# Kernel tuning notes

Hardware: AMD Instinct MI355X
Metric: run time of the kernel (lower is better)

The kernel has to match this reference:

```python
import jax, jax.numpy as jnp
import numpy as np

IN_FEATURES = 4096
OUT_FEATURES = 4096
BATCH = 4096
MASK_DENSITY = 0.05  # typical power-grid neighborhood sparsity


def setup_inputs() -> dict:
    key = jax.random.key(0)
    k_x, k_w, k_b, k_m = jax.random.split(key, 4)
    x = jax.random.normal(k_x, (BATCH, IN_FEATURES), dtype=jnp.float32)
    # kaiming_uniform_(a=sqrt(5)) -> uniform(-bound, bound), bound = sqrt(6/((1+5)*fan_in)) = 1/sqrt(fan_in)
    w_bound = 1.0 / np.sqrt(IN_FEATURES)
    weight = jax.random.uniform(k_w, (OUT_FEATURES, IN_FEATURES), dtype=jnp.float32,
                                minval=-w_bound, maxval=w_bound)
    bias = jax.random.uniform(k_b, (OUT_FEATURES,), dtype=jnp.float32,
                              minval=-w_bound, maxval=w_bound)
    # fixed binary neighborhood filter (non-trainable), int-valued {0,1} as in the torch module
    myFilter = (jax.random.uniform(k_m, (OUT_FEATURES, IN_FEATURES)) < MASK_DENSITY).astype(jnp.float32)
    return {"x": x, "weight": weight, "bias": bias, "myFilter": myFilter}


def reference(x, weight, bias, myFilter):
    # F.linear(input, weight * myFilter, bias): y = x @ (W * M)^T + b
    masked_w = weight * myFilter                      # [out, in]
    return jnp.einsum('bi,oi->bo', x, masked_w) + bias  # [batch, out]
```

## Files before the change

### kernel.cpp

```cpp
#include <hip/hip_runtime.h>
#include <hip/hip_bf16.h>
#include <stdint.h>

#define IN_F   4096
#define OUT_F  4096
#define BATCH  4096

typedef __bf16 bf16x8_t __attribute__((ext_vector_type(8)));
typedef float  f32x4_t  __attribute__((ext_vector_type(4)));
typedef float  f32x4v   __attribute__((ext_vector_type(4)));
typedef unsigned short u16x4v __attribute__((ext_vector_type(4)));

#define AS_GLOBAL(p) ((const __attribute__((address_space(1))) void*)(p))
#define AS_LDS(p)    ((__attribute__((address_space(3))) void*)(p))

__device__ __forceinline__ unsigned short f32_to_bf16_rne(float f) {
    union { float f; uint32_t u; } v; v.f = f;
    uint32_t u = v.u;
    u += 0x7FFFu + ((u >> 16) & 1u);
    return (unsigned short)(u >> 16);
}

__global__ __launch_bounds__(256)
void convert_kernel(const float* __restrict__ x,
                    const float* __restrict__ w,
                    const float* __restrict__ m,
                    unsigned short* __restrict__ xb,
                    unsigned short* __restrict__ wb) {
    const int64_t i0 = (int64_t)blockIdx.x * 512 + threadIdx.x;
#pragma unroll
    for (int u = 0; u < 2; ++u) {
        const int64_t i = i0 + u * 256;
        f32x4v xv = __builtin_nontemporal_load(&((const f32x4v*)x)[i]);
        f32x4v wv = __builtin_nontemporal_load(&((const f32x4v*)w)[i]);
        f32x4v mv = __builtin_nontemporal_load(&((const f32x4v*)m)[i]);
        u16x4v xo, wo;
        xo.x = f32_to_bf16_rne(xv.x);
        xo.y = f32_to_bf16_rne(xv.y);
        xo.z = f32_to_bf16_rne(xv.z);
        xo.w = f32_to_bf16_rne(xv.w);
        wo.x = f32_to_bf16_rne(wv.x * mv.x);
        wo.y = f32_to_bf16_rne(wv.y * mv.y);
        wo.z = f32_to_bf16_rne(wv.z * mv.z);
        wo.w = f32_to_bf16_rne(wv.w * mv.w);
        ((u16x4v*)xb)[i] = xo;
        ((u16x4v*)wb)[i] = wo;
    }
}

#define BM 128
#define BN 128
#define BK 64

__global__ __launch_bounds__(256)
void gemm_bt_bias_kernel(const unsigned short* __restrict__ A,
                         const unsigned short* __restrict__ B,
                         const float* __restrict__ bias,
                         float* __restrict__ C) {
    __shared__ __align__(16) unsigned short sA[2][BM * BK];
    __shared__ __align__(16) unsigned short sB[2][BN * BK];

    const int t    = threadIdx.x;
    const int wv   = t >> 6;
    const int lane = t & 63;
    const int quad = lane >> 4;
    const int l16  = lane & 15;

    const int bm = blockIdx.y * BM;
    const int bn = blockIdx.x * BN;

    const int wr = wv >> 1;
    const int wc = wv & 1;

    const int srow = t >> 3;
    const int scol = 8 * ((t & 7) ^ ((t >> 3) & 7));
    const unsigned short* gA = A + (int64_t)(bm + srow) * IN_F + scol;
    const unsigned short* gB = B + (int64_t)(bn + srow) * IN_F + scol;

#define ISSUE_TILE(buf, k0)                                                   \
    do {                                                                      \
        _Pragma("unroll")                                                     \
        for (int r = 0; r < 4; ++r) {                                         \
            __builtin_amdgcn_global_load_lds(                                 \
                AS_GLOBAL(gA + (int64_t)r * 32 * IN_F + (k0)),                \
                AS_LDS((char*)sA[buf] + r * 4096 + wv * 1024 + lane * 16), 16, 0, 0); \
            __builtin_amdgcn_global_load_lds(                                 \
                AS_GLOBAL(gB + (int64_t)r * 32 * IN_F + (k0)),                \
                AS_LDS((char*)sB[buf] + r * 4096 + wv * 1024 + lane * 16), 16, 0, 0); \
        }                                                                     \
    } while (0)

    f32x4_t acc[4][4];
#pragma unroll
    for (int mi = 0; mi < 4; ++mi)
#pragma unroll
        for (int ni = 0; ni < 4; ++ni)
            acc[mi][ni] = (f32x4_t){0.f, 0.f, 0.f, 0.f};

    ISSUE_TILE(0, 0);

    int buf = 0;
    for (int k0 = 0; k0 < IN_F; k0 += BK, buf ^= 1) {
        __syncthreads();

        if (k0 + BK < IN_F)
            ISSUE_TILE(buf ^ 1, k0 + BK);

        const unsigned short* __restrict__ cA = sA[buf];
        const unsigned short* __restrict__ cB = sB[buf];

#pragma unroll
        for (int ks = 0; ks < 2; ++ks) {
            bf16x8_t af[4], bf[4];
#pragma unroll
            for (int mi = 0; mi < 4; ++mi) {
                const int row = wr * 64 + mi * 16 + l16;
                const int ch  = (ks * 4 + quad) ^ (row & 7);
                af[mi] = *(const bf16x8_t*)(cA + row * BK + ch * 8);
            }
#pragma unroll
            for (int ni = 0; ni < 4; ++ni) {
                const int row = wc * 64 + ni * 16 + l16;
                const int ch  = (ks * 4 + quad) ^ (row & 7);
                bf[ni] = *(const bf16x8_t*)(cB + row * BK + ch * 8);
            }
#pragma unroll
            for (int mi = 0; mi < 4; ++mi)
#pragma unroll
                for (int ni = 0; ni < 4; ++ni)
                    acc[mi][ni] = __builtin_amdgcn_mfma_f32_16x16x32_bf16(
                        af[mi], bf[ni], acc[mi][ni], 0, 0, 0);
        }
    }

    float bv[4];
#pragma unroll
    for (int ni = 0; ni < 4; ++ni)
        bv[ni] = bias[bn + wc * 64 + ni * 16 + l16];

#pragma unroll
    for (int mi = 0; mi < 4; ++mi) {
        const int row0 = bm + wr * 64 + mi * 16 + quad * 4;
#pragma unroll
        for (int ni = 0; ni < 4; ++ni) {
            const int col = bn + wc * 64 + ni * 16 + l16;
#pragma unroll
            for (int reg = 0; reg < 4; ++reg)
                C[(int64_t)(row0 + reg) * OUT_F + col] = acc[mi][ni][reg] + bv[ni];
        }
    }
#undef ISSUE_TILE
}

__global__ void fallback_gemm_kernel(const float* __restrict__ x,
                                     const float* __restrict__ w,
                                     const float* __restrict__ bias,
                                     const float* __restrict__ m,
                                     float* __restrict__ y) {
    __shared__ float sx[16][17];
    __shared__ float sw[16][17];
    const int tx = threadIdx.x, ty = threadIdx.y;
    const int row = blockIdx.y * 16 + ty;
    const int col = blockIdx.x * 16 + tx;
    float acc = 0.f;
    for (int k0 = 0; k0 < IN_F; k0 += 16) {
        sx[ty][tx] = x[(int64_t)row * IN_F + k0 + tx];
        const int64_t widx = (int64_t)(blockIdx.x * 16 + ty) * IN_F + k0 + tx;
        sw[ty][tx] = w[widx] * m[widx];
        __syncthreads();
#pragma unroll
        for (int kk = 0; kk < 16; ++kk)
            acc += sx[ty][kk] * sw[tx][kk];
        __syncthreads();
    }
    y[(int64_t)row * OUT_F + col] = acc + bias[col];
}

extern "C" void kernel_launch(void* const* d_in, const int* in_sizes, int n_in,
                              void* d_out, int out_size, void* d_ws, size_t ws_size,
                              hipStream_t stream) {
    const float* x    = (const float*)d_in[0];
    const float* w    = (const float*)d_in[1];
    const float* bias = (const float*)d_in[2];
    const float* m    = (const float*)d_in[3];
    float* y = (float*)d_out;

    const size_t need = (size_t)2 * (size_t)OUT_F * (size_t)IN_F * sizeof(unsigned short);

    if (ws_size >= need) {
        unsigned short* xb = (unsigned short*)d_ws;
        unsigned short* wb = xb + (size_t)BATCH * IN_F;

        convert_kernel<<<8192, 256, 0, stream>>>(x, w, m, xb, wb);

        dim3 grid(OUT_F / BN, BATCH / BM);
        gemm_bt_bias_kernel<<<grid, 256, 0, stream>>>(xb, wb, bias, y);
    } else {
        dim3 grid(OUT_F / 16, BATCH / 16);
        dim3 block(16, 16);
        fallback_gemm_kernel<<<grid, block, 0, stream>>>(x, w, bias, m, y);
    }
}
```

Measured before the change: 324.0 us.

## Fuse mask-multiply and bf16 conversion into GEMM tile loading

```diff
diff --git a/kernel.cpp b/kernel.cpp
--- a/kernel.cpp
+++ b/kernel.cpp
@@ -8,55 +8,17 @@
 
 typedef __bf16 bf16x8_t __attribute__((ext_vector_type(8)));
 typedef float  f32x4_t  __attribute__((ext_vector_type(4)));
-typedef float  f32x4v   __attribute__((ext_vector_type(4)));
-typedef unsigned short u16x4v __attribute__((ext_vector_type(4)));
-
-#define AS_GLOBAL(p) ((const __attribute__((address_space(1))) void*)(p))
-#define AS_LDS(p)    ((__attribute__((address_space(3))) void*)(p))
-
-__device__ __forceinline__ unsigned short f32_to_bf16_rne(float f) {
-    union { float f; uint32_t u; } v; v.f = f;
-    uint32_t u = v.u;
-    u += 0x7FFFu + ((u >> 16) & 1u);
-    return (unsigned short)(u >> 16);
-}
-
-__global__ __launch_bounds__(256)
-void convert_kernel(const float* __restrict__ x,
-                    const float* __restrict__ w,
-                    const float* __restrict__ m,
-                    unsigned short* __restrict__ xb,
-                    unsigned short* __restrict__ wb) {
-    const int64_t i0 = (int64_t)blockIdx.x * 512 + threadIdx.x;
-#pragma unroll
-    for (int u = 0; u < 2; ++u) {
-        const int64_t i = i0 + u * 256;
-        f32x4v xv = __builtin_nontemporal_load(&((const f32x4v*)x)[i]);
-        f32x4v wv = __builtin_nontemporal_load(&((const f32x4v*)w)[i]);
-        f32x4v mv = __builtin_nontemporal_load(&((const f32x4v*)m)[i]);
-        u16x4v xo, wo;
-        xo.x = f32_to_bf16_rne(xv.x);
-        xo.y = f32_to_bf16_rne(xv.y);
-        xo.z = f32_to_bf16_rne(xv.z);
-        xo.w = f32_to_bf16_rne(xv.w);
-        wo.x = f32_to_bf16_rne(wv.x * mv.x);
-        wo.y = f32_to_bf16_rne(wv.y * mv.y);
-        wo.z = f32_to_bf16_rne(wv.z * mv.z);
-        wo.w = f32_to_bf16_rne(wv.w * mv.w);
-        ((u16x4v*)xb)[i] = xo;
-        ((u16x4v*)wb)[i] = wo;
-    }
-}
 
 #define BM 128
 #define BN 128
 #define BK 64
 
-__global__ __launch_bounds__(256)
-void gemm_bt_bias_kernel(const unsigned short* __restrict__ A,
-                         const unsigned short* __restrict__ B,
-                         const float* __restrict__ bias,
-                         float* __restrict__ C) {
+__global__ __launch_bounds__(256, 2)
+void fused_gemm_kernel(const float* __restrict__ x,
+                       const float* __restrict__ w,
+                       const float* __restrict__ bias,
+                       const float* __restrict__ m,
+                       float* __restrict__ C) {
     __shared__ __align__(16) unsigned short sA[2][BM * BK];
     __shared__ __align__(16) unsigned short sB[2][BN * BK];
 
@@ -66,27 +28,56 @@
     const int quad = lane >> 4;
     const int l16  = lane & 15;
 
-    const int bm = blockIdx.y * BM;
-    const int bn = blockIdx.x * BN;
+    const int bid = blockIdx.x;
+    const int swz = (bid & 7) * 128 + (bid >> 3);
+    const int bx  = swz & 31;
+    const int by  = swz >> 5;
+    const int bm  = by * BM;
+    const int bn  = bx * BN;
 
     const int wr = wv >> 1;
     const int wc = wv & 1;
 
     const int srow = t >> 3;
-    const int scol = 8 * ((t & 7) ^ ((t >> 3) & 7));
-    const unsigned short* gA = A + (int64_t)(bm + srow) * IN_F + scol;
-    const unsigned short* gB = B + (int64_t)(bn + srow) * IN_F + scol;
+    const int c8   = t & 7;
+    const float* gx = x + (int64_t)(bm + srow) * IN_F + c8 * 8;
+    const float* gw = w + (int64_t)(bn + srow) * IN_F + c8 * 8;
+    const float* gm = m + (int64_t)(bn + srow) * IN_F + c8 * 8;
 
-#define ISSUE_TILE(buf, k0)                                                   \
+    const int ldsoff = srow * 128 + ((c8 ^ (srow & 7)) * 16);
+
+    f32x4_t rx[4][2], rw[4][2], rm[4][2];
+
+#define LOAD_TILE(k0)                                                         \
     do {                                                                      \
         _Pragma("unroll")                                                     \
         for (int r = 0; r < 4; ++r) {                                         \
-            __builtin_amdgcn_global_load_lds(                                 \
-                AS_GLOBAL(gA + (int64_t)r * 32 * IN_F + (k0)),                \
-                AS_LDS((char*)sA[buf] + r * 4096 + wv * 1024 + lane * 16), 16, 0, 0); \
-            __builtin_amdgcn_global_load_lds(                                 \
-                AS_GLOBAL(gB + (int64_t)r * 32 * IN_F + (k0)),                \
-                AS_LDS((char*)sB[buf] + r * 4096 + wv * 1024 + lane * 16), 16, 0, 0); \
+            const float* px = gx + (int64_t)r * 32 * IN_F + (k0);             \
+            const float* pw = gw + (int64_t)r * 32 * IN_F + (k0);             \
+            const float* pm = gm + (int64_t)r * 32 * IN_F + (k0);             \
+            rx[r][0] = *(const f32x4_t*)(px);                                 \
+            rx[r][1] = *(const f32x4_t*)(px + 4);                             \
+            rw[r][0] = *(const f32x4_t*)(pw);                                 \
+            rw[r][1] = *(const f32x4_t*)(pw + 4);                             \
+            rm[r][0] = *(const f32x4_t*)(pm);                                 \
+            rm[r][1] = *(const f32x4_t*)(pm + 4);                             \
+        }                                                                     \
+    } while (0)
+
+#define CVT_WRITE(bufi)                                                       \
+    do {                                                                      \
+        _Pragma("unroll")                                                     \
+        for (int r = 0; r < 4; ++r) {                                         \
+            bf16x8_t va, vb;                                                  \
+            _Pragma("unroll")                                                 \
+            for (int j = 0; j < 4; ++j) {                                     \
+                va[j]     = (__bf16)rx[r][0][j];                              \
+                va[j + 4] = (__bf16)rx[r][1][j];                              \
+                vb[j]     = (__bf16)(rw[r][0][j] * rm[r][0][j]);              \
+                vb[j + 4] = (__bf16)(rw[r][1][j] * rm[r][1][j]);              \
+            }                                                                 \
+            *(bf16x8_t*)((char*)sA[bufi] + r * 4096 + ldsoff) = va;           \
+            *(bf16x8_t*)((char*)sB[bufi] + r * 4096 + ldsoff) = vb;           \
         }                                                                     \
     } while (0)
 
@@ -97,21 +88,22 @@
         for (int ni = 0; ni < 4; ++ni)
             acc[mi][ni] = (f32x4_t){0.f, 0.f, 0.f, 0.f};
 
-    ISSUE_TILE(0, 0);
+    LOAD_TILE(0);
+    CVT_WRITE(0);
 
     int buf = 0;
     for (int k0 = 0; k0 < IN_F; k0 += BK, buf ^= 1) {
         __syncthreads();
 
         if (k0 + BK < IN_F)
-            ISSUE_TILE(buf ^ 1, k0 + BK);
+            LOAD_TILE(k0 + BK);
 
         const unsigned short* __restrict__ cA = sA[buf];
         const unsigned short* __restrict__ cB = sB[buf];
 
 #pragma unroll
         for (int ks = 0; ks < 2; ++ks) {
-            bf16x8_t af[4], bf[4];
+            bf16x8_t af[4], bfr[4];
 #pragma unroll
             for (int mi = 0; mi < 4; ++mi) {
                 const int row = wr * 64 + mi * 16 + l16;
@@ -122,15 +114,18 @@
             for (int ni = 0; ni < 4; ++ni) {
                 const int row = wc * 64 + ni * 16 + l16;
                 const int ch  = (ks * 4 + quad) ^ (row & 7);
-                bf[ni] = *(const bf16x8_t*)(cB + row * BK + ch * 8);
+                bfr[ni] = *(const bf16x8_t*)(cB + row * BK + ch * 8);
             }
 #pragma unroll
             for (int mi = 0; mi < 4; ++mi)
 #pragma unroll
                 for (int ni = 0; ni < 4; ++ni)
                     acc[mi][ni] = __builtin_amdgcn_mfma_f32_16x16x32_bf16(
-                        af[mi], bf[ni], acc[mi][ni], 0, 0, 0);
+                        af[mi], bfr[ni], acc[mi][ni], 0, 0, 0);
         }
+
+        if (k0 + BK < IN_F)
+            CVT_WRITE(buf ^ 1);
     }
 
     float bv[4];
@@ -149,31 +144,8 @@
                 C[(int64_t)(row0 + reg) * OUT_F + col] = acc[mi][ni][reg] + bv[ni];
         }
     }
-#undef ISSUE_TILE
-}
-
-__global__ void fallback_gemm_kernel(const float* __restrict__ x,
-                                     const float* __restrict__ w,
-                                     const float* __restrict__ bias,
-                                     const float* __restrict__ m,
-                                     float* __restrict__ y) {
-    __shared__ float sx[16][17];
-    __shared__ float sw[16][17];
-    const int tx = threadIdx.x, ty = threadIdx.y;
-    const int row = blockIdx.y * 16 + ty;
-    const int col = blockIdx.x * 16 + tx;
-    float acc = 0.f;
-    for (int k0 = 0; k0 < IN_F; k0 += 16) {
-        sx[ty][tx] = x[(int64_t)row * IN_F + k0 + tx];
-        const int64_t widx = (int64_t)(blockIdx.x * 16 + ty) * IN_F + k0 + tx;
-        sw[ty][tx] = w[widx] * m[widx];
-        __syncthreads();
-#pragma unroll
-        for (int kk = 0; kk < 16; ++kk)
-            acc += sx[ty][kk] * sw[tx][kk];
-        __syncthreads();
-    }
-    y[(int64_t)row * OUT_F + col] = acc + bias[col];
+#undef LOAD_TILE
+#undef CVT_WRITE
 }
 
 extern "C" void kernel_launch(void* const* d_in, const int* in_sizes, int n_in,
@@ -185,19 +157,7 @@
     const float* m    = (const float*)d_in[3];
     float* y = (float*)d_out;
 
-    const size_t need = (size_t)2 * (size_t)OUT_F * (size_t)IN_F * sizeof(unsigned short);
+    (void)d_ws; (void)ws_size;
 
-    if (ws_size >= need) {
-        unsigned short* xb = (unsigned short*)d_ws;
-        unsigned short* wb = xb + (size_t)BATCH * IN_F;
-
-        convert_kernel<<<8192, 256, 0, stream>>>(x, w, m, xb, wb);
-
-        dim3 grid(OUT_F / BN, BATCH / BM);
-        gemm_bt_bias_kernel<<<grid, 256, 0, stream>>>(xb, wb, bias, y);
-    } else {
-        dim3 grid(OUT_F / 16, BATCH / 16);
-        dim3 block(16, 16);
-        fallback_gemm_kernel<<<grid, block, 0, stream>>>(x, w, bias, m, y);
-    }
+    fused_gemm_kernel<<<1024, 256, 0, stream>>>(x, w, bias, m, y);
 }
```

Measured after the change: 741.7 us. 129% more time.

## Replace GEMM with 256x256-tile 8-wave phased pipeline kernel

Applied to the files above, without the earlier changes.

```diff
diff --git a/kernel.cpp b/kernel.cpp
--- a/kernel.cpp
+++ b/kernel.cpp
@@ -48,89 +48,168 @@
     }
 }
 
-#define BM 128
-#define BN 128
+#define BM 256
+#define BN 256
 #define BK 64
-
-__global__ __launch_bounds__(256)
-void gemm_bt_bias_kernel(const unsigned short* __restrict__ A,
-                         const unsigned short* __restrict__ B,
-                         const float* __restrict__ bias,
-                         float* __restrict__ C) {
-    __shared__ __align__(16) unsigned short sA[2][BM * BK];
-    __shared__ __align__(16) unsigned short sB[2][BN * BK];
+#define NT (IN_F / BK)
+
+__global__ __launch_bounds__(512, 2)
+void gemm_8phase_kernel(const unsigned short* __restrict__ A,
+                        const unsigned short* __restrict__ B,
+                        const float* __restrict__ bias,
+                        float* __restrict__ C) {
+    __shared__ __align__(16) unsigned short sA[2][2][128 * 64];
+    __shared__ __align__(16) unsigned short sB[2][2][128 * 64];
 
     const int t    = threadIdx.x;
     const int wv   = t >> 6;
     const int lane = t & 63;
     const int quad = lane >> 4;
     const int l16  = lane & 15;
-
-    const int bm = blockIdx.y * BM;
-    const int bn = blockIdx.x * BN;
-
-    const int wr = wv >> 1;
-    const int wc = wv & 1;
+    const int wr   = wv >> 2;
+    const int wc   = wv & 3;
+    const int bhalf = wc >> 1;
+    const int brow0 = (wc & 1) * 64;
+
+    const int bid = blockIdx.x;
+    const int swz = (bid & 7) * 32 + (bid >> 3);
+    const int bm  = (swz >> 4) * BM;
+    const int bn  = (swz & 15) * BN;
 
     const int srow = t >> 3;
-    const int scol = 8 * ((t & 7) ^ ((t >> 3) & 7));
+    const int scol = 8 * ((t & 7) ^ (srow & 7));
     const unsigned short* gA = A + (int64_t)(bm + srow) * IN_F + scol;
     const unsigned short* gB = B + (int64_t)(bn + srow) * IN_F + scol;
-
-#define ISSUE_TILE(buf, k0)                                                   \
+    const int ldsoff = t * 16;
+
+#define STAGE_A(TT, h)                                                        \
     do {                                                                      \
         _Pragma("unroll")                                                     \
-        for (int r = 0; r < 4; ++r) {                                         \
+        for (int rr = 0; rr < 2; ++rr)                                        \
             __builtin_amdgcn_global_load_lds(                                 \
-                AS_GLOBAL(gA + (int64_t)r * 32 * IN_F + (k0)),                \
-                AS_LDS((char*)sA[buf] + r * 4096 + wv * 1024 + lane * 16), 16, 0, 0); \
+                AS_GLOBAL(gA + (int64_t)((h) * 128 + rr * 64) * IN_F + (TT) * BK), \
+                AS_LDS((char*)sA[(TT) & 1][h] + rr * 8192 + ldsoff), 16, 0, 0); \
+    } while (0)
+#define STAGE_B(TT, h)                                                        \
+    do {                                                                      \
+        _Pragma("unroll")                                                     \
+        for (int rr = 0; rr < 2; ++rr)                                        \
             __builtin_amdgcn_global_load_lds(                                 \
-                AS_GLOBAL(gB + (int64_t)r * 32 * IN_F + (k0)),                \
-                AS_LDS((char*)sB[buf] + r * 4096 + wv * 1024 + lane * 16), 16, 0, 0); \
-        }                                                                     \
+                AS_GLOBAL(gB + (int64_t)((h) * 128 + rr * 64) * IN_F + (TT) * BK), \
+                AS_LDS((char*)sB[(TT) & 1][h] + rr * 8192 + ldsoff), 16, 0, 0); \
     } while (0)
 
-    f32x4_t acc[4][4];
-#pragma unroll
-    for (int mi = 0; mi < 4; ++mi)
+    f32x4_t acc[8][4];
+#pragma unroll
+    for (int mi = 0; mi < 8; ++mi)
 #pragma unroll
         for (int ni = 0; ni < 4; ++ni)
             acc[mi][ni] = (f32x4_t){0.f, 0.f, 0.f, 0.f};
 
-    ISSUE_TILE(0, 0);
-
-    int buf = 0;
-    for (int k0 = 0; k0 < IN_F; k0 += BK, buf ^= 1) {
-        __syncthreads();
-
-        if (k0 + BK < IN_F)
-            ISSUE_TILE(buf ^ 1, k0 + BK);
-
-        const unsigned short* __restrict__ cA = sA[buf];
-        const unsigned short* __restrict__ cB = sB[buf];
-
-#pragma unroll
-        for (int ks = 0; ks < 2; ++ks) {
-            bf16x8_t af[4], bf[4];
-#pragma unroll
-            for (int mi = 0; mi < 4; ++mi) {
-                const int row = wr * 64 + mi * 16 + l16;
-                const int ch  = (ks * 4 + quad) ^ (row & 7);
-                af[mi] = *(const bf16x8_t*)(cA + row * BK + ch * 8);
-            }
-#pragma unroll
-            for (int ni = 0; ni < 4; ++ni) {
-                const int row = wc * 64 + ni * 16 + l16;
-                const int ch  = (ks * 4 + quad) ^ (row & 7);
-                bf[ni] = *(const bf16x8_t*)(cB + row * BK + ch * 8);
-            }
-#pragma unroll
-            for (int mi = 0; mi < 4; ++mi)
-#pragma unroll
-                for (int ni = 0; ni < 4; ++ni)
+    STAGE_A(0, 0); STAGE_A(0, 1); STAGE_B(0, 0); STAGE_B(0, 1);
+    STAGE_B(1, 0); STAGE_B(1, 1); STAGE_A(1, 0);
+    asm volatile("s_waitcnt vmcnt(6)" ::: "memory");
+    __builtin_amdgcn_s_barrier();
+
+    for (int T = 0; T < NT; ++T) {
+        const unsigned short* myA = sA[T & 1][wr];
+        const unsigned short* myB = sB[T & 1][bhalf];
+
+        bf16x8_t af[4][2], bf0[2][2], bf1[2][2];
+
+#pragma unroll
+        for (int j = 0; j < 4; ++j) {
+            const int row = j * 16 + l16;
+#pragma unroll
+            for (int ks = 0; ks < 2; ++ks)
+                af[j][ks] = *(const bf16x8_t*)(myA + row * 64 +
+                                ((ks * 4 + quad) ^ (row & 7)) * 8);
+        }
+#pragma unroll
+        for (int j = 0; j < 2; ++j) {
+            const int row = brow0 + j * 16 + l16;
+#pragma unroll
+            for (int ks = 0; ks < 2; ++ks)
+                bf0[j][ks] = *(const bf16x8_t*)(myB + row * 64 +
+                                ((ks * 4 + quad) ^ (row & 7)) * 8);
+        }
+        if (T + 1 < NT) STAGE_A(T + 1, 1);
+        __builtin_amdgcn_s_barrier();
+        asm volatile("s_waitcnt lgkmcnt(0)" ::: "memory");
+        __builtin_amdgcn_s_setprio(1);
+#pragma unroll
+        for (int mi = 0; mi < 4; ++mi)
+#pragma unroll
+            for (int ni = 0; ni < 2; ++ni)
+#pragma unroll
+                for (int ks = 0; ks < 2; ++ks)
                     acc[mi][ni] = __builtin_amdgcn_mfma_f32_16x16x32_bf16(
-                        af[mi], bf[ni], acc[mi][ni], 0, 0, 0);
-        }
+                        af[mi][ks], bf0[ni][ks], acc[mi][ni], 0, 0, 0);
+        __builtin_amdgcn_s_setprio(0);
+        __builtin_amdgcn_s_barrier();
+
+#pragma unroll
+        for (int j = 0; j < 2; ++j) {
+            const int row = brow0 + (j + 2) * 16 + l16;
+#pragma unroll
+            for (int ks = 0; ks < 2; ++ks)
+                bf1[j][ks] = *(const bf16x8_t*)(myB + row * 64 +
+                                ((ks * 4 + quad) ^ (row & 7)) * 8);
+        }
+        __builtin_amdgcn_s_barrier();
+        asm volatile("s_waitcnt lgkmcnt(0)" ::: "memory");
+        __builtin_amdgcn_s_setprio(1);
+#pragma unroll
+        for (int mi = 0; mi < 4; ++mi)
+#pragma unroll
+            for (int ni = 0; ni < 2; ++ni)
+#pragma unroll
+                for (int ks = 0; ks < 2; ++ks)
+                    acc[mi][ni + 2] = __builtin_amdgcn_mfma_f32_16x16x32_bf16(
+                        af[mi][ks], bf1[ni][ks], acc[mi][ni + 2], 0, 0, 0);
+        __builtin_amdgcn_s_setprio(0);
+        __builtin_amdgcn_s_barrier();
+
+#pragma unroll
+        for (int j = 0; j < 4; ++j) {
+            const int row = (j + 4) * 16 + l16;
+#pragma unroll
+            for (int ks = 0; ks < 2; ++ks)
+                af[j][ks] = *(const bf16x8_t*)(myA + row * 64 +
+                                ((ks * 4 + quad) ^ (row & 7)) * 8);
+        }
+        if (T + 2 < NT) STAGE_B(T + 2, 0);
+        __builtin_amdgcn_s_barrier();
+        asm volatile("s_waitcnt lgkmcnt(0)" ::: "memory");
+        __builtin_amdgcn_s_setprio(1);
+#pragma unroll
+        for (int mi = 0; mi < 4; ++mi)
+#pragma unroll
+            for (int ni = 0; ni < 2; ++ni)
+#pragma unroll
+                for (int ks = 0; ks < 2; ++ks)
+                    acc[mi + 4][ni + 2] = __builtin_amdgcn_mfma_f32_16x16x32_bf16(
+                        af[mi][ks], bf1[ni][ks], acc[mi + 4][ni + 2], 0, 0, 0);
+        __builtin_amdgcn_s_setprio(0);
+        __builtin_amdgcn_s_barrier();
+
+        if (T + 2 < NT) { STAGE_B(T + 2, 1); STAGE_A(T + 2, 0); }
+        __builtin_amdgcn_s_barrier();
+        __builtin_amdgcn_s_setprio(1);
+#pragma unroll
+        for (int mi = 0; mi < 4; ++mi)
+#pragma unroll
+            for (int ni = 0; ni < 2; ++ni)
+#pragma unroll
+                for (int ks = 0; ks < 2; ++ks)
+                    acc[mi + 4][ni] = __builtin_amdgcn_mfma_f32_16x16x32_bf16(
+                        af[mi][ks], bf0[ni][ks], acc[mi + 4][ni], 0, 0, 0);
+        __builtin_amdgcn_s_setprio(0);
+        if (T < NT - 2)
+            asm volatile("s_waitcnt vmcnt(6)" ::: "memory");
+        else if (T < NT - 1)
+            asm volatile("s_waitcnt vmcnt(0)" ::: "memory");
+        __builtin_amdgcn_s_barrier();
     }
 
     float bv[4];
@@ -139,8 +218,8 @@
         bv[ni] = bias[bn + wc * 64 + ni * 16 + l16];
 
 #pragma unroll
-    for (int mi = 0; mi < 4; ++mi) {
-        const int row0 = bm + wr * 64 + mi * 16 + quad * 4;
+    for (int mi = 0; mi < 8; ++mi) {
+        const int row0 = bm + wr * 128 + mi * 16 + quad * 4;
 #pragma unroll
         for (int ni = 0; ni < 4; ++ni) {
             const int col = bn + wc * 64 + ni * 16 + l16;
@@ -149,7 +228,8 @@
                 C[(int64_t)(row0 + reg) * OUT_F + col] = acc[mi][ni][reg] + bv[ni];
         }
     }
-#undef ISSUE_TILE
+#undef STAGE_A
+#undef STAGE_B
 }
 
 __global__ void fallback_gemm_kernel(const float* __restrict__ x,
@@ -193,8 +273,7 @@
 
         convert_kernel<<<8192, 256, 0, stream>>>(x, w, m, xb, wb);
 
-        dim3 grid(OUT_F / BN, BATCH / BM);
-        gemm_bt_bias_kernel<<<grid, 256, 0, stream>>>(xb, wb, bias, y);
+        gemm_8phase_kernel<<<256, 512, 0, stream>>>(xb, wb, bias, y);
     } else {
         dim3 grid(OUT_F / 16, BATCH / 16);
         dim3 block(16, 16);
```

Measured after the change: 326.7 us. No clear change (+0.8%).
